# Kernel tuning notes

Measured on AMD Instinct MI355X. Metric: run time of the kernel, lower is better.

## Reference

```python
import jax, jax.numpy as jnp
import numpy as np

B, G, D = 16, 20000, 64   # batch, num_genes, feature_dim
S, L = 500, 128           # num_gene_sets, max genes per set (padded)


def setup_inputs() -> dict:
    key = jax.random.key(0)
    k1, k2, k3 = jax.random.split(key, 3)
    gene_features = jax.random.normal(k1, (B, G, D), dtype=jnp.float32)
    geneset_indices = jax.random.randint(k2, (S, L), 0, G, dtype=jnp.int32)
    set_mask = jnp.ones((S, L), dtype=bool)  # all positions valid (uniform-size sets)
    attn_weights = jax.random.normal(k3, (S, L, D), dtype=jnp.float32)
    return {
        "gene_features": gene_features,
        "attn_weights": attn_weights,
        "geneset_indices": geneset_indices,
        "set_mask": set_mask,
    }


def reference(gene_features, attn_weights, geneset_indices, set_mask):
    # Gather per-set gene features: [B, S, L, D]
    gathered = jnp.take(gene_features, geneset_indices, axis=1)
    # Masked softmax over the set-member axis L (independent per feature dim),
    # matching F.softmax(attention_weights, dim=1) per gene set.
    neg = jnp.finfo(attn_weights.dtype).min
    logits = jnp.where(set_mask[:, :, None], attn_weights, neg)  # [S, L, D]
    attn = jax.nn.softmax(logits, axis=1)                        # [S, L, D]
    # Weighted sum over set members -> [B, S, D]
    return jnp.einsum('bsld,sld->bsd', gathered, attn)
```

## Files before the change

### kernel.cpp

```cpp
#include <hip/hip_runtime.h>
#include <math.h>


#define NB 16
#define NG 20000
#define ND 64
#define NS 500
#define NL 128

typedef unsigned short ushortx8 __attribute__((ext_vector_type(8)));
typedef float floatx8 __attribute__((ext_vector_type(8)));

__device__ __forceinline__ float bf2f(unsigned short u) {
    union { unsigned int i; float f; } x;
    x.i = ((unsigned int)u) << 16;
    return x.f;
}

__device__ __forceinline__ unsigned short f2bf(float f) {
    union { float f; unsigned int i; } x;
    x.f = f;
    unsigned int r = x.i + 0x7FFFu + ((x.i >> 16) & 1u);
    return (unsigned short)(r >> 16);
}

__global__ void detect_dtype_kernel(const unsigned short* __restrict__ aw,
                                    int* __restrict__ flag) {
    const unsigned int e = ((unsigned int)aw[2 * threadIdx.x] >> 7) & 0xFFu;
    const unsigned long long m = __ballot(e >= 100u && e <= 135u);
    if (threadIdx.x == 0) *flag = (__popcll(m) >= 32) ? 1 : 0;
}

template<bool BF16>
__global__ __launch_bounds__(1024)
void agg_kernel(const void* __restrict__ gf_,
                const void* __restrict__ aw_,
                const int*  __restrict__ idx,
                void*       __restrict__ out_,
                const int*  __restrict__ flag)
{
    if (*flag != (BF16 ? 1 : 0)) return;

    __shared__ float attn_s[NL * ND];
    __shared__ float red[16 * ND];
    __shared__ float inv_sum[ND];
    __shared__ int   gidx[NL];

    const int s = blockIdx.x;
    const int t = threadIdx.x;

    if (t < NL) gidx[t] = idx[s * NL + t];

    const int d    = t & 63;
    const int part = t >> 6;
    const unsigned short* awp = (const unsigned short*)aw_ + (size_t)s * (NL * ND);

    float m = -INFINITY;
    #pragma unroll
    for (int i = 0; i < 8; ++i) {
        const int l = part * 8 + i;
        const float v = BF16 ? bf2f(awp[l * ND + d])
                             : ((const float*)aw_)[(size_t)s * (NL * ND) + l * ND + d];
        attn_s[l * ND + d] = v;
        m = fmaxf(m, v);
    }
    red[part * ND + d] = m;
    __syncthreads();
    float m_all = -INFINITY;
    #pragma unroll
    for (int p = 0; p < 16; ++p) m_all = fmaxf(m_all, red[p * ND + d]);
    __syncthreads();

    float psum = 0.f;
    #pragma unroll
    for (int i = 0; i < 8; ++i) {
        const int l = part * 8 + i;
        const float e = __expf(attn_s[l * ND + d] - m_all);
        attn_s[l * ND + d] = e;
        psum += e;
    }
    red[part * ND + d] = psum;
    __syncthreads();
    if (part == 0) {
        float tot = 0.f;
        #pragma unroll
        for (int p = 0; p < 16; ++p) tot += red[p * ND + d];
        inv_sum[d] = 1.0f / tot;
    }
    __syncthreads();

    const int b    = t >> 6;
    const int lane = t & 63;
    const int lp   = lane >> 3;
    const int q    = lane & 7;
    const int d0   = q * 8;

    float acc[8];
    #pragma unroll
    for (int j = 0; j < 8; ++j) acc[j] = 0.f;

    if (BF16) {
        const char* gbase = (const char*)gf_ + (size_t)b * (NG * ND * 2) + d0 * 2;
        #pragma unroll 4
        for (int k = 0; k < 16; ++k) {
            const int l = lp * 16 + k;
            const int g = gidx[l];
            const ushortx8 u = *(const ushortx8*)(gbase + (size_t)g * (ND * 2));
            const floatx8  w = *(const floatx8*)&attn_s[l * ND + d0];
            #pragma unroll
            for (int j = 0; j < 8; ++j) acc[j] += bf2f(u[j]) * w[j];
        }
    } else {
        const char* gbase = (const char*)gf_ + (size_t)b * (NG * ND * 4) + d0 * 4;
        #pragma unroll 4
        for (int k = 0; k < 16; ++k) {
            const int l = lp * 16 + k;
            const int g = gidx[l];
            const floatx8 u = *(const floatx8*)(gbase + (size_t)g * (ND * 4));
            const floatx8 w = *(const floatx8*)&attn_s[l * ND + d0];
            #pragma unroll
            for (int j = 0; j < 8; ++j) acc[j] += u[j] * w[j];
        }
    }

    #pragma unroll
    for (int j = 0; j < 8; ++j) {
        acc[j] += __shfl_xor(acc[j], 8);
        acc[j] += __shfl_xor(acc[j], 16);
        acc[j] += __shfl_xor(acc[j], 32);
    }

    if (lp == 0) {
        const floatx8 inv = *(const floatx8*)&inv_sum[d0];
        if (BF16) {
            ushortx8 o;
            #pragma unroll
            for (int j = 0; j < 8; ++j) o[j] = f2bf(acc[j] * inv[j]);
            *(ushortx8*)((unsigned short*)out_ + ((size_t)b * NS + s) * ND + d0) = o;
        } else {
            floatx8 o;
            #pragma unroll
            for (int j = 0; j < 8; ++j) o[j] = acc[j] * inv[j];
            *(floatx8*)((float*)out_ + ((size_t)b * NS + s) * ND + d0) = o;
        }
    }
}

extern "C" void kernel_launch(void* const* d_in, const int* in_sizes, int n_in,
                              void* d_out, int out_size, void* d_ws, size_t ws_size,
                              hipStream_t stream) {
    const void* gf  = d_in[0];
    const void* aw  = d_in[1];
    const int*  idx = (const int*)d_in[2];
    int* flag = (int*)d_ws;

    detect_dtype_kernel<<<1, 64, 0, stream>>>((const unsigned short*)aw, flag);
    agg_kernel<true ><<<NS, 1024, 0, stream>>>(gf, aw, idx, d_out, flag);
    agg_kernel<false><<<NS, 1024, 0, stream>>>(gf, aw, idx, d_out, flag);
}
```

Before: 150.7 us.

## Prefetch gathered gene rows during softmax and drop redundant barriers

Issues the first batch of gathered gene-feature loads into registers before the softmax exp pass, then software-pipelines the remaining gathers a fixed distance ahead in the accumulation loop. The block-wide sum-reduction step and one barrier are removed; each output lane now sums the partial denominators itself. __syncthreads is replaced by an LDS-only waitcnt plus s_barrier so outstanding global loads are not drained at barriers. This hides gather latency behind the softmax work, at the cost of more registers per thread under a 1024-thread block and redundant denominator sums.

```diff
diff --git a/kernel.cpp b/kernel.cpp
--- a/kernel.cpp
+++ b/kernel.cpp
@@ -24,6 +24,11 @@
     return (unsigned short)(r >> 16);
 }
 
+__device__ __forceinline__ void lgkm_barrier() {
+    asm volatile("s_waitcnt lgkmcnt(0)" ::: "memory");
+    __builtin_amdgcn_s_barrier();
+}
+
 __global__ void detect_dtype_kernel(const unsigned short* __restrict__ aw,
                                     int* __restrict__ flag) {
     const unsigned int e = ((unsigned int)aw[2 * threadIdx.x] >> 7) & 0xFFu;
@@ -43,7 +48,6 @@
 
     __shared__ float attn_s[NL * ND];
     __shared__ float red[16 * ND];
-    __shared__ float inv_sum[ND];
     __shared__ int   gidx[NL];
 
     const int s = blockIdx.x;
@@ -65,11 +69,37 @@
         m = fmaxf(m, v);
     }
     red[part * ND + d] = m;
-    __syncthreads();
+    lgkm_barrier();
+
     float m_all = -INFINITY;
     #pragma unroll
     for (int p = 0; p < 16; ++p) m_all = fmaxf(m_all, red[p * ND + d]);
-    __syncthreads();
+
+    const int b    = t >> 6;
+    const int lane = t & 63;
+    const int lp   = lane >> 3;
+    const int q    = lane & 7;
+    const int d0   = q * 8;
+
+    ushortx8 ub[8];
+    floatx8  uf[4];
+    if (BF16) {
+        const unsigned short* gb = (const unsigned short*)gf_ + (size_t)b * (NG * ND) + d0;
+        #pragma unroll
+        for (int k = 0; k < 8; ++k) {
+            const int g = gidx[lp * 16 + k];
+            ub[k] = *(const ushortx8*)(gb + (size_t)g * ND);
+        }
+    } else {
+        const float* gb = (const float*)gf_ + (size_t)b * (NG * ND) + d0;
+        #pragma unroll
+        for (int k = 0; k < 4; ++k) {
+            const int g = gidx[lp * 16 + k];
+            uf[k] = *(const floatx8*)(gb + (size_t)g * ND);
+        }
+    }
+
+    lgkm_barrier();
 
     float psum = 0.f;
     #pragma unroll
@@ -80,46 +110,39 @@
         psum += e;
     }
     red[part * ND + d] = psum;
-    __syncthreads();
-    if (part == 0) {
-        float tot = 0.f;
-        #pragma unroll
-        for (int p = 0; p < 16; ++p) tot += red[p * ND + d];
-        inv_sum[d] = 1.0f / tot;
-    }
-    __syncthreads();
-
-    const int b    = t >> 6;
-    const int lane = t & 63;
-    const int lp   = lane >> 3;
-    const int q    = lane & 7;
-    const int d0   = q * 8;
+    lgkm_barrier();
 
     float acc[8];
     #pragma unroll
     for (int j = 0; j < 8; ++j) acc[j] = 0.f;
 
     if (BF16) {
-        const char* gbase = (const char*)gf_ + (size_t)b * (NG * ND * 2) + d0 * 2;
-        #pragma unroll 4
+        const unsigned short* gb = (const unsigned short*)gf_ + (size_t)b * (NG * ND) + d0;
+        #pragma unroll
         for (int k = 0; k < 16; ++k) {
             const int l = lp * 16 + k;
-            const int g = gidx[l];
-            const ushortx8 u = *(const ushortx8*)(gbase + (size_t)g * (ND * 2));
-            const floatx8  w = *(const floatx8*)&attn_s[l * ND + d0];
+            const floatx8  w  = *(const floatx8*)&attn_s[l * ND + d0];
+            const ushortx8 uk = ub[k & 7];
+            if (k + 8 < 16) {
+                const int g = gidx[lp * 16 + k + 8];
+                ub[k & 7] = *(const ushortx8*)(gb + (size_t)g * ND);
+            }
             #pragma unroll
-            for (int j = 0; j < 8; ++j) acc[j] += bf2f(u[j]) * w[j];
+            for (int j = 0; j < 8; ++j) acc[j] += bf2f(uk[j]) * w[j];
         }
     } else {
-        const char* gbase = (const char*)gf_ + (size_t)b * (NG * ND * 4) + d0 * 4;
-        #pragma unroll 4
+        const float* gb = (const float*)gf_ + (size_t)b * (NG * ND) + d0;
+        #pragma unroll
         for (int k = 0; k < 16; ++k) {
             const int l = lp * 16 + k;
-            const int g = gidx[l];
-            const floatx8 u = *(const floatx8*)(gbase + (size_t)g * (ND * 4));
-            const floatx8 w = *(const floatx8*)&attn_s[l * ND + d0];
+            const floatx8 w  = *(const floatx8*)&attn_s[l * ND + d0];
+            const floatx8 uk = uf[k & 3];
+            if (k + 4 < 16) {
+                const int g = gidx[lp * 16 + k + 4];
+                uf[k & 3] = *(const floatx8*)(gb + (size_t)g * ND);
+            }
             #pragma unroll
-            for (int j = 0; j < 8; ++j) acc[j] += u[j] * w[j];
+            for (int j = 0; j < 8; ++j) acc[j] += uk[j] * w[j];
         }
     }
 
@@ -131,16 +154,20 @@
     }
 
     if (lp == 0) {
-        const floatx8 inv = *(const floatx8*)&inv_sum[d0];
+        floatx8 tot;
+        #pragma unroll
+        for (int j = 0; j < 8; ++j) tot[j] = 0.f;
+        #pragma unroll
+        for (int p = 0; p < 16; ++p) tot += *(const floatx8*)&red[p * ND + d0];
         if (BF16) {
             ushortx8 o;
             #pragma unroll
-            for (int j = 0; j < 8; ++j) o[j] = f2bf(acc[j] * inv[j]);
+            for (int j = 0; j < 8; ++j) o[j] = f2bf(acc[j] * (1.0f / tot[j]));
             *(ushortx8*)((unsigned short*)out_ + ((size_t)b * NS + s) * ND + d0) = o;
         } else {
             floatx8 o;
             #pragma unroll
-            for (int j = 0; j < 8; ++j) o[j] = acc[j] * inv[j];
+            for (int j = 0; j < 8; ++j) o[j] = acc[j] * (1.0f / tot[j]);
             *(floatx8*)((float*)out_ + ((size_t)b * NS + s) * ND + d0) = o;
         }
     }
```

After: 158.2 us. +4.9%, slower.

## Stream gathered fp32 gene rows into LDS with async global_load_lds ring buffer

Applied to the files above, without the earlier changes.

The fp32 path now gathers gene-feature rows with global_load_lds into a 6-deep per-wave LDS ring, using explicit vmcnt waits. Loads are issued before the softmax exponent phase so gather latency overlaps the softmax math. Barriers become raw lgkmcnt waits plus s_barrier, and the final normalisation reads the shared partial sums directly, dropping one barrier and the inv_sum array. Each block's static LDS use grows by about 96KB, which could limit occupancy, and correctness depends on the hand-written waitcnt ordering.

```diff
diff --git a/kernel.cpp b/kernel.cpp
--- a/kernel.cpp
+++ b/kernel.cpp
@@ -22,6 +22,11 @@
     x.f = f;
     unsigned int r = x.i + 0x7FFFu + ((x.i >> 16) & 1u);
     return (unsigned short)(r >> 16);
+}
+
+__device__ __forceinline__ void lgkm_barrier() {
+    asm volatile("s_waitcnt lgkmcnt(0)" ::: "memory");
+    __builtin_amdgcn_s_barrier();
 }
 
 __global__ void detect_dtype_kernel(const unsigned short* __restrict__ aw,
@@ -43,8 +48,8 @@
 
     __shared__ float attn_s[NL * ND];
     __shared__ float red[16 * ND];
-    __shared__ float inv_sum[ND];
     __shared__ int   gidx[NL];
+    __shared__ __align__(16) char stage[16 * 6 * 1024];
 
     const int s = blockIdx.x;
     const int t = threadIdx.x;
@@ -65,11 +70,38 @@
         m = fmaxf(m, v);
     }
     red[part * ND + d] = m;
-    __syncthreads();
+    lgkm_barrier();
+
     float m_all = -INFINITY;
     #pragma unroll
     for (int p = 0; p < 16; ++p) m_all = fmaxf(m_all, red[p * ND + d]);
-    __syncthreads();
+
+    const int b    = t >> 6;
+    const int lane = t & 63;
+
+    const int r  = lane >> 4;
+    const int dq = lane & 15;
+
+    char* stage_w = &stage[b * 6144];
+    const float* gfp = (const float*)gf_ + (size_t)b * (NG * ND) + dq * 4;
+
+#define GL_ISSUE(i) do {                                                      \
+        const int g_ = gidx[4 * (i) + r];                                     \
+        const float* s_ = gfp + (size_t)g_ * ND;                              \
+        __builtin_amdgcn_global_load_lds(                                     \
+            (const __attribute__((address_space(1))) unsigned int*)s_,        \
+            (__attribute__((address_space(3))) unsigned int*)                 \
+                (stage_w + ((i) % 6) * 1024),                                 \
+            16, 0, 0);                                                        \
+    } while (0)
+
+    if (!BF16) {
+        asm volatile("s_waitcnt vmcnt(0)" ::: "memory");
+        GL_ISSUE(0); GL_ISSUE(1); GL_ISSUE(2);
+        GL_ISSUE(3); GL_ISSUE(4); GL_ISSUE(5);
+    }
+
+    lgkm_barrier();
 
     float psum = 0.f;
     #pragma unroll
@@ -80,70 +112,91 @@
         psum += e;
     }
     red[part * ND + d] = psum;
-    __syncthreads();
-    if (part == 0) {
-        float tot = 0.f;
+    lgkm_barrier();
+
+    if (!BF16) {
+        float a0 = 0.f, a1 = 0.f, a2 = 0.f, a3 = 0.f;
+
+#define CONSUME(i, cnt) do {                                                  \
+            asm volatile("s_waitcnt vmcnt(" #cnt ")" ::: "memory");           \
+            __builtin_amdgcn_sched_barrier(0);                                \
+            const float4 u_ = *(const float4*)(stage_w + ((i) % 6) * 1024     \
+                                               + lane * 16);                  \
+            const float4 w_ = *(const float4*)                                \
+                &attn_s[(4 * (i) + r) * ND + dq * 4];                         \
+            asm volatile("s_waitcnt lgkmcnt(0)" ::: "memory");                \
+            __builtin_amdgcn_sched_barrier(0);                                \
+            if ((i) + 6 < 32) GL_ISSUE((i) + 6);                              \
+            a0 += u_.x * w_.x; a1 += u_.y * w_.y;                             \
+            a2 += u_.z * w_.z; a3 += u_.w * w_.w;                             \
+        } while (0)
+
+        CONSUME(0, 5);   CONSUME(1, 5);   CONSUME(2, 5);   CONSUME(3, 5);
+        CONSUME(4, 5);   CONSUME(5, 5);   CONSUME(6, 5);   CONSUME(7, 5);
+        CONSUME(8, 5);   CONSUME(9, 5);   CONSUME(10, 5);  CONSUME(11, 5);
+        CONSUME(12, 5);  CONSUME(13, 5);  CONSUME(14, 5);  CONSUME(15, 5);
+        CONSUME(16, 5);  CONSUME(17, 5);  CONSUME(18, 5);  CONSUME(19, 5);
+        CONSUME(20, 5);  CONSUME(21, 5);  CONSUME(22, 5);  CONSUME(23, 5);
+        CONSUME(24, 5);  CONSUME(25, 5);  CONSUME(26, 5);  CONSUME(27, 4);
+        CONSUME(28, 3);  CONSUME(29, 2);  CONSUME(30, 1);  CONSUME(31, 0);
+#undef CONSUME
+
+        a0 += __shfl_xor(a0, 16); a0 += __shfl_xor(a0, 32);
+        a1 += __shfl_xor(a1, 16); a1 += __shfl_xor(a1, 32);
+        a2 += __shfl_xor(a2, 16); a2 += __shfl_xor(a2, 32);
+        a3 += __shfl_xor(a3, 16); a3 += __shfl_xor(a3, 32);
+
+        if (lane < 16) {
+            float t0 = 0.f, t1 = 0.f, t2 = 0.f, t3 = 0.f;
+            #pragma unroll
+            for (int p = 0; p < 16; ++p) {
+                const float4 v = *(const float4*)&red[p * ND + dq * 4];
+                t0 += v.x; t1 += v.y; t2 += v.z; t3 += v.w;
+            }
+            float4 o;
+            o.x = a0 / t0; o.y = a1 / t1; o.z = a2 / t2; o.w = a3 / t3;
+            *(float4*)((float*)out_ + ((size_t)b * NS + s) * ND + dq * 4) = o;
+        }
+    } else {
+        const int lp = lane >> 3;
+        const int q  = lane & 7;
+        const int d0 = q * 8;
+
+        float acc[8];
         #pragma unroll
-        for (int p = 0; p < 16; ++p) tot += red[p * ND + d];
-        inv_sum[d] = 1.0f / tot;
-    }
-    __syncthreads();
-
-    const int b    = t >> 6;
-    const int lane = t & 63;
-    const int lp   = lane >> 3;
-    const int q    = lane & 7;
-    const int d0   = q * 8;
-
-    float acc[8];
-    #pragma unroll
-    for (int j = 0; j < 8; ++j) acc[j] = 0.f;
-
-    if (BF16) {
-        const char* gbase = (const char*)gf_ + (size_t)b * (NG * ND * 2) + d0 * 2;
+        for (int j = 0; j < 8; ++j) acc[j] = 0.f;
+
+        const unsigned short* gb = (const unsigned short*)gf_ + (size_t)b * (NG * ND) + d0;
         #pragma unroll 4
         for (int k = 0; k < 16; ++k) {
             const int l = lp * 16 + k;
             const int g = gidx[l];
-            const ushortx8 u = *(const ushortx8*)(gbase + (size_t)g * (ND * 2));
+            const ushortx8 u = *(const ushortx8*)(gb + (size_t)g * ND);
             const floatx8  w = *(const floatx8*)&attn_s[l * ND + d0];
             #pragma unroll
             for (int j = 0; j < 8; ++j) acc[j] += bf2f(u[j]) * w[j];
         }
-    } else {
-        const char* gbase = (const char*)gf_ + (size_t)b * (NG * ND * 4) + d0 * 4;
-        #pragma unroll 4
-        for (int k = 0; k < 16; ++k) {
-            const int l = lp * 16 + k;
-            const int g = gidx[l];
-            const floatx8 u = *(const floatx8*)(gbase + (size_t)g * (ND * 4));
-            const floatx8 w = *(const floatx8*)&attn_s[l * ND + d0];
-            #pragma unroll
-            for (int j = 0; j < 8; ++j) acc[j] += u[j] * w[j];
-        }
-    }
-
-    #pragma unroll
-    for (int j = 0; j < 8; ++j) {
-        acc[j] += __shfl_xor(acc[j], 8);
-        acc[j] += __shfl_xor(acc[j], 16);
-        acc[j] += __shfl_xor(acc[j], 32);
-    }
-
-    if (lp == 0) {
-        const floatx8 inv = *(const floatx8*)&inv_sum[d0];
-        if (BF16) {
+
+        #pragma unroll
+        for (int j = 0; j < 8; ++j) {
+            acc[j] += __shfl_xor(acc[j], 8);
+            acc[j] += __shfl_xor(acc[j], 16);
+            acc[j] += __shfl_xor(acc[j], 32);
+        }
+
+        if (lp == 0) {
+            floatx8 tot;
+            #pragma unroll
+            for (int j = 0; j < 8; ++j) tot[j] = 0.f;
+            #pragma unroll
+            for (int p = 0; p < 16; ++p) tot += *(const floatx8*)&red[p * ND + d0];
             ushortx8 o;
             #pragma unroll
-            for (int j = 0; j < 8; ++j) o[j] = f2bf(acc[j] * inv[j]);
+            for (int j = 0; j < 8; ++j) o[j] = f2bf(acc[j] * (1.0f / tot[j]));
             *(ushortx8*)((unsigned short*)out_ + ((size_t)b * NS + s) * ND + d0) = o;
-        } else {
-            floatx8 o;
-            #pragma unroll
-            for (int j = 0; j < 8; ++j) o[j] = acc[j] * inv[j];
-            *(floatx8*)((float*)out_ + ((size_t)b * NS + s) * ND + d0) = o;
-        }
-    }
+        }
+    }
+#undef GL_ISSUE
 }
 
 extern "C" void kernel_launch(void* const* d_in, const int* in_sizes, int n_in,
```

Result: slower. 153.8 us (+2.1%).
